# Optimization experiments

Measured on AMD Instinct MI355X. Metric: run time of the kernel, lower is better.

The kernel has to match this reference:

```python
import jax, jax.numpy as jnp
import numpy as np

N, E, XD, H, L, G, C = 20000, 320000, 128, 256, 4, 128, 10
EPS = 1e-5


def setup_inputs() -> dict:
    key = jax.random.key(0)
    ks = jax.random.split(key, 24)
    s = 0.05
    inp = {
        "x": jax.random.normal(ks[0], (N, XD), jnp.float32),
        "edge_index": jax.random.randint(ks[1], (2, E), 0, N, jnp.int32),
        "batch": jnp.sort(jax.random.randint(ks[2], (N,), 0, G, jnp.int32)),
        "encW": jax.random.normal(ks[3], (XD, H), jnp.float32) * s,
        "encB": jnp.zeros((H,), jnp.float32),
        "convW": jax.random.normal(ks[4], (L, H, H), jnp.float32) * s,
        "convB": jnp.zeros((L, H), jnp.float32),
        "bnG": jnp.ones((L, H), jnp.float32),
        "bnB": jnp.zeros((L, H), jnp.float32),
        "fcW1": jax.random.normal(ks[5], (H, H), jnp.float32) * s,
        "fcB1": jnp.zeros((H,), jnp.float32),
        "fcG1": jnp.ones((H,), jnp.float32),
        "fcBe1": jnp.zeros((H,), jnp.float32),
        "fcW2": jax.random.normal(ks[6], (H, H), jnp.float32) * s,
        "fcB2": jnp.zeros((H,), jnp.float32),
        "fcG2": jnp.ones((H,), jnp.float32),
        "fcBe2": jnp.zeros((H,), jnp.float32),
        "fcW3": jax.random.normal(ks[7], (H, C), jnp.float32) * s,
        "fcB3": jnp.zeros((C,), jnp.float32),
    }
    return inp


def _bn(h, g, b):
    # BatchNorm1d, training-mode batch statistics (biased var), eps=1e-5
    m = h.mean(0)
    v = h.var(0)
    return g * (h - m) * jax.lax.rsqrt(v + EPS) + b


def _forward(x, edge_index, batch, encW, encB, convW, convB, bnG, bnB,
             fcW1, fcB1, fcG1, fcBe1, fcW2, fcB2, fcG2, fcBe2, fcW3, fcB3):
    src, dst = edge_index[0], edge_index[1]
    # GCN symmetric normalization with implicit self-loops (fill value 1)
    deg = jax.ops.segment_sum(jnp.ones((E,), x.dtype), dst, num_segments=N) + 1.0
    dinv = jax.lax.rsqrt(deg)
    enorm = (dinv[src] * dinv[dst])[:, None]       # [E,1]
    self_norm = (dinv * dinv)[:, None]             # [N,1] self-loop coeff

    h = x @ encW + encB                            # node encoder
    for i in range(L):
        t = h @ convW[i]                           # GCNConv linear (no bias)
        agg = jax.ops.segment_sum(t[src] * enorm, dst, num_segments=N)
        t = agg + t * self_norm + convB[i]         # aggregate + self loop + bias
        h = jax.nn.relu(_bn(t, bnG[i], bnB[i]))    # dropout is identity (eval)

    # global mean pool over graph ids
    sums = jax.ops.segment_sum(h, batch, num_segments=G)
    cnts = jax.ops.segment_sum(jnp.ones((N,), h.dtype), batch, num_segments=G)
    g = sums / jnp.maximum(cnts, 1.0)[:, None]     # [G,H]

    # fc_out: MLP(Linear->BN->ReLU->Linear) -> BN -> Linear
    m = jax.nn.relu(_bn(g @ fcW1 + fcB1, fcG1, fcBe1)) @ fcW2 + fcB2
    m = _bn(m, fcG2, fcBe2)
    return m @ fcW3 + fcB3                         # [G,C]


def reference(x, edge_index, batch, encW, encB, convW, convB, bnG, bnB,
              fcW1, fcB1, fcG1, fcBe1, fcW2, fcB2, fcG2, fcBe2, fcW3, fcB3):
    return _forward(x, edge_index, batch, encW, encB, convW, convB, bnG, bnB,
                    fcW1, fcB1, fcG1, fcBe1, fcW2, fcB2, fcG2, fcBe2, fcW3, fcB3)
```

## Files before the change

### kernel.cpp

```cpp
#include <hip/hip_runtime.h>
#include <hip/hip_bf16.h>
#include <cstddef>

#define N_NODES 20000
#define N_EDGES 320000
#define XDIM 128
#define H 256
#define LAYERS 4
#define G_GRAPHS 128
#define C_OUT 10
#define EPS_BN 1e-5f
#define NSLOT 64
#define NB 8

typedef __attribute__((ext_vector_type(8))) short short8;
typedef __attribute__((ext_vector_type(4))) float f32x4;
typedef __attribute__((address_space(3))) unsigned int lds_u32;
typedef const __attribute__((address_space(1))) unsigned int glob_u32;

__global__ void hist_kernel(const int* __restrict__ dst, int* __restrict__ cnt, int E) {
    int e = blockIdx.x * blockDim.x + threadIdx.x;
    if (e < E) atomicAdd(&cnt[dst[e]], 1);
}

__global__ void scan_kernel(const int* __restrict__ cnt, int* __restrict__ rowstart,
                            float* __restrict__ dinv, int N) {
    __shared__ int partial[1024];
    int tid = threadIdx.x;
    int chunk = (N + 1023) / 1024;
    int start = tid * chunk;
    int lsum = 0;
    for (int i = 0; i < chunk; ++i) {
        int idx = start + i;
        if (idx < N) {
            int c = cnt[idx];
            dinv[idx] = 1.0f / sqrtf((float)c + 1.0f);
            lsum += c;
        }
    }
    partial[tid] = lsum;
    __syncthreads();
    for (int off = 1; off < 1024; off <<= 1) {
        int v = (tid >= off) ? partial[tid - off] : 0;
        __syncthreads();
        partial[tid] += v;
        __syncthreads();
    }
    int run = (tid == 0) ? 0 : partial[tid - 1];
    for (int i = 0; i < chunk; ++i) {
        int idx = start + i;
        if (idx < N) { rowstart[idx] = run; run += cnt[idx]; }
    }
    if (tid == 1023) rowstart[N] = partial[1023];
}

__global__ void fill_kernel(const int* __restrict__ src, const int* __restrict__ dst,
                            const int* __restrict__ rowstart, int* __restrict__ cursor,
                            const float* __restrict__ dinv,
                            int* __restrict__ csr_src, float* __restrict__ csr_w, int E) {
    int e = blockIdx.x * blockDim.x + threadIdx.x;
    if (e < E) {
        int s = src[e], d = dst[e];
        int pos = rowstart[d] + atomicAdd(&cursor[d], 1);
        csr_src[pos] = s;
        csr_w[pos] = dinv[s] * dinv[d];
    }
}

__global__ void cast_bf16_kernel(const float* __restrict__ in, __hip_bfloat16* __restrict__ out, int n) {
    int i = blockIdx.x * blockDim.x + threadIdx.x;
    if (i < n) out[i] = __float2bfloat16(in[i]);
}

__global__ void tcast_kernel(const float* __restrict__ in, __hip_bfloat16* __restrict__ out,
                             int R, int C, int layers) {
    int i = blockIdx.x * blockDim.x + threadIdx.x;
    int per = R * C;
    if (i >= per * layers) return;
    int l = i / per, rem = i - l * per;
    int r = rem / C, c = rem - r * C;
    out[(size_t)l * per + (size_t)c * R + r] = __float2bfloat16(in[i]);
}

__device__ __forceinline__ short bf16bits(float x) {
    __hip_bfloat16 b = __float2bfloat16(x);
    return *(short*)&b;
}

template <int K, bool FUSE_BN>
__global__ __launch_bounds__(256) void gemm_bf16_kernel(
    const void* __restrict__ Ain,
    const __hip_bfloat16* __restrict__ BT,
    const float* __restrict__ bias,
    const float* __restrict__ bnsc,
    const float* __restrict__ bnsh,
    __hip_bfloat16* __restrict__ Cbf,
    int M, int Nn) {
    __shared__ short As[64 * 32];
    __shared__ short Bs[128 * 32];
    const short* Ash = (const short*)Ain;
    const float* Af = (const float*)Ain;
    const short* Bsh = (const short*)BT;
    int tid = threadIdx.x;
    int lane = tid & 63;
    int wave = tid >> 6;
    int quad = lane >> 4;
    int lr = lane & 15;
    int wm = (wave & 1) * 32;
    int wn = (wave >> 1) * 64;
    int Mblk = blockIdx.x * 64;
    int Nblk = blockIdx.y * 128;

    f32x4 acc[2][4];
#pragma unroll
    for (int i = 0; i < 2; ++i)
#pragma unroll
        for (int j = 0; j < 4; ++j) acc[i][j] = (f32x4){0.f, 0.f, 0.f, 0.f};

    int srow = tid >> 2, sqs = tid & 3;
    int sqg = sqs ^ ((srow >> 1) & 3);
    int arow = Mblk + srow; if (arow >= M) arow = M - 1;
    int s1 = 256 + tid;
    int brow0 = Nblk + (tid >> 2);
    int qg0 = sqg;
    int brow1 = Nblk + (s1 >> 2);
    int qg1 = (s1 & 3) ^ (((s1 >> 2) >> 1) & 3);

    for (int k0 = 0; k0 < K; k0 += 32) {
        int kc = k0 + sqg * 8;
        __builtin_amdgcn_global_load_lds((glob_u32*)(Bsh + (size_t)brow0 * K + k0 + qg0 * 8),
                                         (lds_u32*)Bs + wave * 256, 16, 0, 0);
        __builtin_amdgcn_global_load_lds((glob_u32*)(Bsh + (size_t)brow1 * K + k0 + qg1 * 8),
                                         (lds_u32*)Bs + 1024 + wave * 256, 16, 0, 0);
        if (FUSE_BN) {
            float4 v0 = *(const float4*)(Af + (size_t)arow * K + kc);
            float4 v1 = *(const float4*)(Af + (size_t)arow * K + kc + 4);
            float4 c0 = *(const float4*)(bnsc + kc);
            float4 c1 = *(const float4*)(bnsc + kc + 4);
            float4 h0 = *(const float4*)(bnsh + kc);
            float4 h1 = *(const float4*)(bnsh + kc + 4);
            short8 pk;
            pk[0] = bf16bits(fmaxf(v0.x * c0.x + h0.x, 0.f));
            pk[1] = bf16bits(fmaxf(v0.y * c0.y + h0.y, 0.f));
            pk[2] = bf16bits(fmaxf(v0.z * c0.z + h0.z, 0.f));
            pk[3] = bf16bits(fmaxf(v0.w * c0.w + h0.w, 0.f));
            pk[4] = bf16bits(fmaxf(v1.x * c1.x + h1.x, 0.f));
            pk[5] = bf16bits(fmaxf(v1.y * c1.y + h1.y, 0.f));
            pk[6] = bf16bits(fmaxf(v1.z * c1.z + h1.z, 0.f));
            pk[7] = bf16bits(fmaxf(v1.w * c1.w + h1.w, 0.f));
            *(short8*)&As[srow * 32 + sqs * 8] = pk;
        } else {
            __builtin_amdgcn_global_load_lds((glob_u32*)(Ash + (size_t)arow * K + kc),
                                             (lds_u32*)As + wave * 256, 16, 0, 0);
        }
        __syncthreads();
        short8 af[2], bfr[4];
#pragma unroll
        for (int mi = 0; mi < 2; ++mi) {
            int r = wm + mi * 16 + lr;
            af[mi] = *(const short8*)&As[r * 32 + (quad ^ ((r >> 1) & 3)) * 8];
        }
#pragma unroll
        for (int ni = 0; ni < 4; ++ni) {
            int r = wn + ni * 16 + lr;
            bfr[ni] = *(const short8*)&Bs[r * 32 + (quad ^ ((r >> 1) & 3)) * 8];
        }
#pragma unroll
        for (int mi = 0; mi < 2; ++mi)
#pragma unroll
            for (int ni = 0; ni < 4; ++ni)
                acc[mi][ni] = __builtin_amdgcn_mfma_f32_16x16x32_bf16(af[mi], bfr[ni], acc[mi][ni], 0, 0, 0);
        __syncthreads();
    }
#pragma unroll
    for (int mi = 0; mi < 2; ++mi) {
#pragma unroll
        for (int r = 0; r < 4; ++r) {
            int m = Mblk + wm + mi * 16 + quad * 4 + r;
            if (m < M) {
#pragma unroll
                for (int ni = 0; ni < 4; ++ni) {
                    int n = Nblk + wn + ni * 16 + lr;
                    float v = acc[mi][ni][r];
                    if (bias) v += bias[n];
                    Cbf[(size_t)m * Nn + n] = __float2bfloat16(v);
                }
            }
        }
    }
}

__global__ __launch_bounds__(256) void agg_kernel(const __hip_bfloat16* __restrict__ t,
                           const int* __restrict__ rowstart,
                           const int* __restrict__ csr_src,
                           const float* __restrict__ csr_w,
                           const float* __restrict__ dinv,
                           const float* __restrict__ convB,
                           float* __restrict__ out,
                           float* __restrict__ spart,
                           int N) {
    __shared__ float red[4][256];
    int tid = threadIdx.x;
    int wave = tid >> 6;
    int lane = tid & 63;
    int sub = lane >> 5;
    int hl = lane & 31;
    int stream = wave * 2 + sub;
    int c0 = hl * 8;
    const ushort* tp = (const ushort*)t;
    float sv = 0.f, sq = 0.f;
    int n0 = blockIdx.x * NB;
#pragma unroll 1
    for (int it = 0; it < NB; ++it) {
        int n = n0 + it;
        int s = rowstart[n], e = rowstart[n + 1];
        float a[8] = {};
#pragma unroll 1
        for (int j0 = s; j0 < e; j0 += 16) {
#pragma unroll
            for (int u = 0; u < 2; ++u) {
                int j = j0 + u * 8 + stream;
                int idx = n; float w = 0.f;
                if (j < e) { idx = csr_src[j]; w = csr_w[j]; }
                uint4 v = *(const uint4*)(tp + (size_t)idx * H + c0);
                a[0] += __uint_as_float(v.x << 16) * w;
                a[1] += __uint_as_float(v.x & 0xffff0000u) * w;
                a[2] += __uint_as_float(v.y << 16) * w;
                a[3] += __uint_as_float(v.y & 0xffff0000u) * w;
                a[4] += __uint_as_float(v.z << 16) * w;
                a[5] += __uint_as_float(v.z & 0xffff0000u) * w;
                a[6] += __uint_as_float(v.w << 16) * w;
                a[7] += __uint_as_float(v.w & 0xffff0000u) * w;
            }
        }
#pragma unroll
        for (int k = 0; k < 8; ++k) a[k] += __shfl_xor(a[k], 32);
        if (sub == 0) {
            *(float4*)&red[wave][c0] = make_float4(a[0], a[1], a[2], a[3]);
            *(float4*)&red[wave][c0 + 4] = make_float4(a[4], a[5], a[6], a[7]);
        }
        __syncthreads();
        int c = tid;
        float val = red[0][c] + red[1][c] + red[2][c] + red[3][c];
        float dn = dinv[n];
        val += __bfloat162float(t[(size_t)n * H + c]) * (dn * dn) + convB[c];
        out[(size_t)n * H + c] = val;
        sv += val; sq += val * val;
        __syncthreads();
    }
    float* sp = spart + (size_t)(blockIdx.x & (NSLOT - 1)) * (2 * H);
    atomicAdd(&sp[tid], sv);
    atomicAdd(&sp[H + tid], sq);
}

__global__ void make_bnparams_kernel(const float* __restrict__ spart,
                                     const float* __restrict__ gamma,
                                     const float* __restrict__ beta,
                                     float* __restrict__ sc, float* __restrict__ sh) {
    int c = threadIdx.x;
    float s = 0.f, s2 = 0.f;
#pragma unroll 8
    for (int i = 0; i < NSLOT; ++i) {
        s  += spart[(size_t)i * (2 * H) + c];
        s2 += spart[(size_t)i * (2 * H) + H + c];
    }
    float invN = 1.0f / (float)N_NODES;
    float mean = s * invN;
    float var = s2 * invN - mean * mean;
    float k = gamma[c] / sqrtf(var + EPS_BN);
    sc[c] = k;
    sh[c] = beta[c] - mean * k;
}

__global__ __launch_bounds__(256) void pool_kernel(const float* __restrict__ t2,
                            const int* __restrict__ batch,
                            const float* __restrict__ sc, const float* __restrict__ sh,
                            float* __restrict__ g, int N) {
    __shared__ float4 red[4][64];
    int gid = blockIdx.x;
    int lo = 0, hi = N;
    while (lo < hi) { int mid = (lo + hi) >> 1; if (batch[mid] < gid) lo = mid + 1; else hi = mid; }
    int s = lo;
    lo = s; hi = N;
    while (lo < hi) { int mid = (lo + hi) >> 1; if (batch[mid] < gid + 1) lo = mid + 1; else hi = mid; }
    int e = lo;
    int wave = threadIdx.x >> 6;
    int lane = threadIdx.x & 63;
    float4 scv = *(const float4*)(sc + lane * 4);
    float4 shv = *(const float4*)(sh + lane * 4);
    float a0 = 0.f, a1 = 0.f, a2 = 0.f, a3 = 0.f;
    for (int r = s + wave; r < e; r += 4) {
        float4 v = *(const float4*)(t2 + (size_t)r * H + lane * 4);
        a0 += __bfloat162float(__float2bfloat16(fmaxf(v.x * scv.x + shv.x, 0.f)));
        a1 += __bfloat162float(__float2bfloat16(fmaxf(v.y * scv.y + shv.y, 0.f)));
        a2 += __bfloat162float(__float2bfloat16(fmaxf(v.z * scv.z + shv.z, 0.f)));
        a3 += __bfloat162float(__float2bfloat16(fmaxf(v.w * scv.w + shv.w, 0.f)));
    }
    red[wave][lane] = make_float4(a0, a1, a2, a3);
    __syncthreads();
    int c = threadIdx.x;
    const float* rf = (const float*)red;
    float sum = rf[c] + rf[256 + c] + rf[512 + c] + rf[768 + c];
    g[(size_t)gid * H + c] = sum / fmaxf((float)(e - s), 1.0f);
}

template <int K, int NN>
__global__ __launch_bounds__(256) void fc_lds_kernel(const float* __restrict__ in,
                                                     const float* __restrict__ W,
                                                     const float* __restrict__ b,
                                                     float* __restrict__ out) {
    __shared__ float row[K];
    int g = blockIdx.x;
    for (int k = threadIdx.x; k < K; k += 256) row[k] = in[(size_t)g * K + k];
    __syncthreads();
    int hc = threadIdx.x;
    if (hc < NN) {
        float acc = b[hc];
#pragma unroll
        for (int k = 0; k < K; ++k) acc += row[k] * W[k * NN + hc];
        out[(size_t)g * NN + hc] = acc;
    }
}

__global__ void fc_out_kernel(const float* __restrict__ in, const float* __restrict__ W,
                              const float* __restrict__ b, float* __restrict__ out) {
    int t = blockIdx.x * blockDim.x + threadIdx.x;
    if (t >= G_GRAPHS * C_OUT) return;
    int g = t / C_OUT, c = t % C_OUT;
    float acc = b[c];
#pragma unroll 16
    for (int k = 0; k < H; ++k) acc += in[(size_t)g * H + k] * W[k * C_OUT + c];
    out[t] = acc;
}

__global__ void bn_head_kernel(const float* __restrict__ in, const float* __restrict__ gamma,
                               const float* __restrict__ beta, float* __restrict__ out,
                               int Grows, int relu) {
    int c = blockIdx.x;
    int r = threadIdx.x;
    __shared__ float red[G_GRAPHS];
    float v = in[r * H + c];
    red[r] = v;
    __syncthreads();
    for (int off = G_GRAPHS / 2; off > 0; off >>= 1) {
        if (r < off) red[r] += red[r + off];
        __syncthreads();
    }
    float mean = red[0] / (float)Grows;
    __syncthreads();
    float d = v - mean;
    red[r] = d * d;
    __syncthreads();
    for (int off = G_GRAPHS / 2; off > 0; off >>= 1) {
        if (r < off) red[r] += red[r + off];
        __syncthreads();
    }
    float var = red[0] / (float)Grows;
    float y = gamma[c] * d / sqrtf(var + EPS_BN) + beta[c];
    if (relu) y = fmaxf(y, 0.f);
    out[r * H + c] = y;
}

extern "C" void kernel_launch(void* const* d_in, const int* in_sizes, int n_in,
                              void* d_out, int out_size, void* d_ws, size_t ws_size,
                              hipStream_t stream) {
    const float* x     = (const float*)d_in[0];
    const int*   edge  = (const int*)d_in[1];
    const int*   batch = (const int*)d_in[2];
    const float* encW  = (const float*)d_in[3];
    const float* encB  = (const float*)d_in[4];
    const float* convW = (const float*)d_in[5];
    const float* convB = (const float*)d_in[6];
    const float* bnG   = (const float*)d_in[7];
    const float* bnB   = (const float*)d_in[8];
    const float* fcW1  = (const float*)d_in[9];
    const float* fcB1  = (const float*)d_in[10];
    const float* fcG1  = (const float*)d_in[11];
    const float* fcBe1 = (const float*)d_in[12];
    const float* fcW2  = (const float*)d_in[13];
    const float* fcB2  = (const float*)d_in[14];
    const float* fcG2  = (const float*)d_in[15];
    const float* fcBe2 = (const float*)d_in[16];
    const float* fcW3  = (const float*)d_in[17];
    const float* fcB3  = (const float*)d_in[18];
    float* out = (float*)d_out;

    const int* srcIdx = edge;
    const int* dstIdx = edge + N_EDGES;

    char* base = (char*)d_ws;
    size_t off = 0;
    auto alloc = [&](size_t bytes) -> void* {
        void* p = base + off;
        off = (off + bytes + 255) & ~(size_t)255;
        return p;
    };
    int*   cnt      = (int*)alloc(N_NODES * 4);
    int*   cursor   = (int*)alloc(N_NODES * 4);
    int*   rowstart = (int*)alloc((N_NODES + 1) * 4);
    float* dinv     = (float*)alloc(N_NODES * 4);
    int*   csr_src  = (int*)alloc(N_EDGES * 4);
    float* csr_w    = (float*)alloc(N_EDGES * 4);
    float* spart    = (float*)alloc((size_t)LAYERS * NSLOT * 2 * H * 4);
    float* scbuf    = (float*)alloc((size_t)LAYERS * H * 4);
    float* shbuf    = (float*)alloc((size_t)LAYERS * H * 4);
    __hip_bfloat16* xbf    = (__hip_bfloat16*)alloc((size_t)N_NODES * XDIM * 2);
    __hip_bfloat16* encWT  = (__hip_bfloat16*)alloc((size_t)H * XDIM * 2);
    __hip_bfloat16* convWT = (__hip_bfloat16*)alloc((size_t)LAYERS * H * H * 2);
    __hip_bfloat16* hbf    = (__hip_bfloat16*)alloc((size_t)N_NODES * H * 2);
    __hip_bfloat16* tbf    = (__hip_bfloat16*)alloc((size_t)N_NODES * H * 2);
    float* t2buf = (float*)alloc((size_t)N_NODES * H * 4);
    float* gpool = (float*)alloc(G_GRAPHS * H * 4);
    float* m1    = (float*)alloc(G_GRAPHS * H * 4);
    float* m2    = (float*)alloc(G_GRAPHS * H * 4);

    hipMemsetAsync(cnt, 0, (size_t)((char*)rowstart - (char*)cnt), stream);
    hipMemsetAsync(spart, 0, (size_t)LAYERS * NSLOT * 2 * H * 4, stream);

    hist_kernel<<<(N_EDGES + 255) / 256, 256, 0, stream>>>(dstIdx, cnt, N_EDGES);
    scan_kernel<<<1, 1024, 0, stream>>>(cnt, rowstart, dinv, N_NODES);
    fill_kernel<<<(N_EDGES + 255) / 256, 256, 0, stream>>>(srcIdx, dstIdx, rowstart, cursor,
                                                           dinv, csr_src, csr_w, N_EDGES);

    cast_bf16_kernel<<<(N_NODES * XDIM + 255) / 256, 256, 0, stream>>>(x, xbf, N_NODES * XDIM);
    tcast_kernel<<<(XDIM * H + 255) / 256, 256, 0, stream>>>(encW, encWT, XDIM, H, 1);
    tcast_kernel<<<(LAYERS * H * H + 255) / 256, 256, 0, stream>>>(convW, convWT, H, H, LAYERS);

    dim3 gridG((N_NODES + 63) / 64, H / 128);
    gemm_bf16_kernel<XDIM, false><<<gridG, 256, 0, stream>>>(
        xbf, encWT, encB, nullptr, nullptr, hbf, N_NODES, H);

    for (int l = 0; l < LAYERS; ++l) {
        float* spartL = spart + (size_t)l * NSLOT * 2 * H;
        if (l == 0) {
            gemm_bf16_kernel<H, false><<<gridG, 256, 0, stream>>>(
                hbf, convWT + (size_t)l * H * H, nullptr, nullptr, nullptr, tbf, N_NODES, H);
        } else {
            gemm_bf16_kernel<H, true><<<gridG, 256, 0, stream>>>(
                t2buf, convWT + (size_t)l * H * H, nullptr,
                scbuf + (size_t)(l - 1) * H, shbuf + (size_t)(l - 1) * H, tbf, N_NODES, H);
        }
        agg_kernel<<<N_NODES / NB, 256, 0, stream>>>(tbf, rowstart, csr_src, csr_w, dinv,
                                                     convB + l * H, t2buf, spartL, N_NODES);
        make_bnparams_kernel<<<1, H, 0, stream>>>(spartL, bnG + l * H, bnB + l * H,
                                                  scbuf + (size_t)l * H, shbuf + (size_t)l * H);
    }

    pool_kernel<<<G_GRAPHS, 256, 0, stream>>>(t2buf, batch,
                                              scbuf + (size_t)(LAYERS - 1) * H,
                                              shbuf + (size_t)(LAYERS - 1) * H, gpool, N_NODES);

    fc_lds_kernel<H, H><<<G_GRAPHS, 256, 0, stream>>>(gpool, fcW1, fcB1, m1);
    bn_head_kernel<<<H, G_GRAPHS, 0, stream>>>(m1, fcG1, fcBe1, m1, G_GRAPHS, 1);
    fc_lds_kernel<H, H><<<G_GRAPHS, 256, 0, stream>>>(m1, fcW2, fcB2, m2);
    bn_head_kernel<<<H, G_GRAPHS, 0, stream>>>(m2, fcG2, fcBe2, m2, G_GRAPHS, 0);
    fc_out_kernel<<<(G_GRAPHS * C_OUT + 255) / 256, 256, 0, stream>>>(m2, fcW3, fcB3, out);
}
```

Before: 453.4 us.

## Double-buffer GEMM tiles, fold BN-param computation into consumers, merge cast kernels

The GEMM now uses two LDS buffers so the next K-tile's global loads are issued before the current tile's MFMAs, with one barrier per iteration instead of two. The separate make_bnparams kernel is removed: each GEMM block and pool block recomputes the BN scale and shift from the partial sums into shared memory. The three cast/transpose kernels are merged into one prep launch. Together these cut launch count and load latency, at the cost of redundant per-block reduction work over NSLOT partials and doubled LDS use.

```diff
diff --git a/kernel.cpp b/kernel.cpp
--- a/kernel.cpp
+++ b/kernel.cpp
@@ -67,19 +67,27 @@
     }
 }
 
-__global__ void cast_bf16_kernel(const float* __restrict__ in, __hip_bfloat16* __restrict__ out, int n) {
+__global__ void prep_kernel(const float* __restrict__ x, const float* __restrict__ encW,
+                            const float* __restrict__ convW,
+                            __hip_bfloat16* __restrict__ xbf,
+                            __hip_bfloat16* __restrict__ encWT,
+                            __hip_bfloat16* __restrict__ convWT) {
     int i = blockIdx.x * blockDim.x + threadIdx.x;
-    if (i < n) out[i] = __float2bfloat16(in[i]);
-}
-
-__global__ void tcast_kernel(const float* __restrict__ in, __hip_bfloat16* __restrict__ out,
-                             int R, int C, int layers) {
-    int i = blockIdx.x * blockDim.x + threadIdx.x;
-    int per = R * C;
-    if (i >= per * layers) return;
-    int l = i / per, rem = i - l * per;
-    int r = rem / C, c = rem - r * C;
-    out[(size_t)l * per + (size_t)c * R + r] = __float2bfloat16(in[i]);
+    const int nx = N_NODES * XDIM;
+    const int ne = XDIM * H;
+    const int nc = LAYERS * H * H;
+    if (i < nx) {
+        xbf[i] = __float2bfloat16(x[i]);
+    } else if (i < nx + ne) {
+        int j = i - nx;
+        int r = j / H, c = j - r * H;
+        encWT[c * XDIM + r] = __float2bfloat16(encW[j]);
+    } else if (i < nx + ne + nc) {
+        int j = i - nx - ne;
+        int l = j / (H * H), rem = j - l * (H * H);
+        int r = rem / H, c = rem - r * H;
+        convWT[(size_t)l * H * H + c * H + r] = __float2bfloat16(convW[j]);
+    }
 }
 
 __device__ __forceinline__ short bf16bits(float x) {
@@ -92,12 +100,15 @@
     const void* __restrict__ Ain,
     const __hip_bfloat16* __restrict__ BT,
     const float* __restrict__ bias,
-    const float* __restrict__ bnsc,
-    const float* __restrict__ bnsh,
+    const float* __restrict__ spart,
+    const float* __restrict__ gamma,
+    const float* __restrict__ beta,
     __hip_bfloat16* __restrict__ Cbf,
     int M, int Nn) {
-    __shared__ short As[64 * 32];
-    __shared__ short Bs[128 * 32];
+    __shared__ short As[2][64 * 32];
+    __shared__ short Bs[2][128 * 32];
+    __shared__ float scs[H];
+    __shared__ float shs[H];
     const short* Ash = (const short*)Ain;
     const float* Af = (const float*)Ain;
     const short* Bsh = (const short*)BT;
@@ -126,51 +137,85 @@
     int brow1 = Nblk + (s1 >> 2);
     int qg1 = (s1 & 3) ^ (((s1 >> 2) >> 1) & 3);
 
-    for (int k0 = 0; k0 < K; k0 += 32) {
+    if (FUSE_BN) {
+        int c = tid;
+        float s = 0.f, s2 = 0.f;
+#pragma unroll 8
+        for (int i = 0; i < NSLOT; ++i) {
+            s  += spart[(size_t)i * (2 * H) + c];
+            s2 += spart[(size_t)i * (2 * H) + H + c];
+        }
+        float invN = 1.0f / (float)N_NODES;
+        float mean = s * invN;
+        float var = s2 * invN - mean * mean;
+        float kk = gamma[c] / sqrtf(var + EPS_BN);
+        scs[c] = kk;
+        shs[c] = beta[c] - mean * kk;
+        __syncthreads();
+    }
+
+    float4 ra0, ra1;
+    auto loadA_f = [&](int k0) {
         int kc = k0 + sqg * 8;
+        ra0 = *(const float4*)(Af + (size_t)arow * K + kc);
+        ra1 = *(const float4*)(Af + (size_t)arow * K + kc + 4);
+    };
+    auto storeA_f = [&](int buf, int k0) {
+        int kc = k0 + sqg * 8;
+        float4 c0 = *(const float4*)&scs[kc];
+        float4 c1 = *(const float4*)&scs[kc + 4];
+        float4 h0 = *(const float4*)&shs[kc];
+        float4 h1 = *(const float4*)&shs[kc + 4];
+        short8 pk;
+        pk[0] = bf16bits(fmaxf(ra0.x * c0.x + h0.x, 0.f));
+        pk[1] = bf16bits(fmaxf(ra0.y * c0.y + h0.y, 0.f));
+        pk[2] = bf16bits(fmaxf(ra0.z * c0.z + h0.z, 0.f));
+        pk[3] = bf16bits(fmaxf(ra0.w * c0.w + h0.w, 0.f));
+        pk[4] = bf16bits(fmaxf(ra1.x * c1.x + h1.x, 0.f));
+        pk[5] = bf16bits(fmaxf(ra1.y * c1.y + h1.y, 0.f));
+        pk[6] = bf16bits(fmaxf(ra1.z * c1.z + h1.z, 0.f));
+        pk[7] = bf16bits(fmaxf(ra1.w * c1.w + h1.w, 0.f));
+        *(short8*)&As[buf][srow * 32 + sqs * 8] = pk;
+    };
+    auto stageA_async = [&](int buf, int k0) {
+        __builtin_amdgcn_global_load_lds((glob_u32*)(Ash + (size_t)arow * K + k0 + sqg * 8),
+                                         (lds_u32*)&As[buf][0] + wave * 256, 16, 0, 0);
+    };
+    auto stageB = [&](int buf, int k0) {
         __builtin_amdgcn_global_load_lds((glob_u32*)(Bsh + (size_t)brow0 * K + k0 + qg0 * 8),
-                                         (lds_u32*)Bs + wave * 256, 16, 0, 0);
+                                         (lds_u32*)&Bs[buf][0] + wave * 256, 16, 0, 0);
         __builtin_amdgcn_global_load_lds((glob_u32*)(Bsh + (size_t)brow1 * K + k0 + qg1 * 8),
-                                         (lds_u32*)Bs + 1024 + wave * 256, 16, 0, 0);
-        if (FUSE_BN) {
-            float4 v0 = *(const float4*)(Af + (size_t)arow * K + kc);
-            float4 v1 = *(const float4*)(Af + (size_t)arow * K + kc + 4);
-            float4 c0 = *(const float4*)(bnsc + kc);
-            float4 c1 = *(const float4*)(bnsc + kc + 4);
-            float4 h0 = *(const float4*)(bnsh + kc);
-            float4 h1 = *(const float4*)(bnsh + kc + 4);
-            short8 pk;
-            pk[0] = bf16bits(fmaxf(v0.x * c0.x + h0.x, 0.f));
-            pk[1] = bf16bits(fmaxf(v0.y * c0.y + h0.y, 0.f));
-            pk[2] = bf16bits(fmaxf(v0.z * c0.z + h0.z, 0.f));
-            pk[3] = bf16bits(fmaxf(v0.w * c0.w + h0.w, 0.f));
-            pk[4] = bf16bits(fmaxf(v1.x * c1.x + h1.x, 0.f));
-            pk[5] = bf16bits(fmaxf(v1.y * c1.y + h1.y, 0.f));
-            pk[6] = bf16bits(fmaxf(v1.z * c1.z + h1.z, 0.f));
-            pk[7] = bf16bits(fmaxf(v1.w * c1.w + h1.w, 0.f));
-            *(short8*)&As[srow * 32 + sqs * 8] = pk;
-        } else {
-            __builtin_amdgcn_global_load_lds((glob_u32*)(Ash + (size_t)arow * K + kc),
-                                             (lds_u32*)As + wave * 256, 16, 0, 0);
-        }
-        __syncthreads();
+                                         (lds_u32*)&Bs[buf][0] + 1024 + wave * 256, 16, 0, 0);
+    };
+
+    constexpr int NK = K / 32;
+    if (FUSE_BN) loadA_f(0); else stageA_async(0, 0);
+    stageB(0, 0);
+#pragma unroll
+    for (int k = 0; k < NK; ++k) {
+        int buf = k & 1;
+        if (FUSE_BN) storeA_f(buf, k * 32);
+        __syncthreads();
+        if (k + 1 < NK) {
+            if (FUSE_BN) loadA_f((k + 1) * 32); else stageA_async(buf ^ 1, (k + 1) * 32);
+            stageB(buf ^ 1, (k + 1) * 32);
+        }
         short8 af[2], bfr[4];
 #pragma unroll
         for (int mi = 0; mi < 2; ++mi) {
             int r = wm + mi * 16 + lr;
-            af[mi] = *(const short8*)&As[r * 32 + (quad ^ ((r >> 1) & 3)) * 8];
+            af[mi] = *(const short8*)&As[buf][r * 32 + (quad ^ ((r >> 1) & 3)) * 8];
         }
 #pragma unroll
         for (int ni = 0; ni < 4; ++ni) {
             int r = wn + ni * 16 + lr;
-            bfr[ni] = *(const short8*)&Bs[r * 32 + (quad ^ ((r >> 1) & 3)) * 8];
+            bfr[ni] = *(const short8*)&Bs[buf][r * 32 + (quad ^ ((r >> 1) & 3)) * 8];
         }
 #pragma unroll
         for (int mi = 0; mi < 2; ++mi)
 #pragma unroll
             for (int ni = 0; ni < 4; ++ni)
                 acc[mi][ni] = __builtin_amdgcn_mfma_f32_16x16x32_bf16(af[mi], bfr[ni], acc[mi][ni], 0, 0, 0);
-        __syncthreads();
     }
 #pragma unroll
     for (int mi = 0; mi < 2; ++mi) {
@@ -253,30 +298,31 @@
     atomicAdd(&sp[H + tid], sq);
 }
 
-__global__ void make_bnparams_kernel(const float* __restrict__ spart,
-                                     const float* __restrict__ gamma,
-                                     const float* __restrict__ beta,
-                                     float* __restrict__ sc, float* __restrict__ sh) {
-    int c = threadIdx.x;
-    float s = 0.f, s2 = 0.f;
-#pragma unroll 8
-    for (int i = 0; i < NSLOT; ++i) {
-        s  += spart[(size_t)i * (2 * H) + c];
-        s2 += spart[(size_t)i * (2 * H) + H + c];
-    }
-    float invN = 1.0f / (float)N_NODES;
-    float mean = s * invN;
-    float var = s2 * invN - mean * mean;
-    float k = gamma[c] / sqrtf(var + EPS_BN);
-    sc[c] = k;
-    sh[c] = beta[c] - mean * k;
-}
-
 __global__ __launch_bounds__(256) void pool_kernel(const float* __restrict__ t2,
                             const int* __restrict__ batch,
-                            const float* __restrict__ sc, const float* __restrict__ sh,
+                            const float* __restrict__ spart,
+                            const float* __restrict__ gamma,
+                            const float* __restrict__ beta,
                             float* __restrict__ g, int N) {
     __shared__ float4 red[4][64];
+    __shared__ float scs[H];
+    __shared__ float shs[H];
+    {
+        int c = threadIdx.x;
+        float s = 0.f, s2 = 0.f;
+#pragma unroll 8
+        for (int i = 0; i < NSLOT; ++i) {
+            s  += spart[(size_t)i * (2 * H) + c];
+            s2 += spart[(size_t)i * (2 * H) + H + c];
+        }
+        float invN = 1.0f / (float)N_NODES;
+        float mean = s * invN;
+        float var = s2 * invN - mean * mean;
+        float kk = gamma[c] / sqrtf(var + EPS_BN);
+        scs[c] = kk;
+        shs[c] = beta[c] - mean * kk;
+    }
+    __syncthreads();
     int gid = blockIdx.x;
     int lo = 0, hi = N;
     while (lo < hi) { int mid = (lo + hi) >> 1; if (batch[mid] < gid) lo = mid + 1; else hi = mid; }
@@ -286,8 +332,8 @@
     int e = lo;
     int wave = threadIdx.x >> 6;
     int lane = threadIdx.x & 63;
-    float4 scv = *(const float4*)(sc + lane * 4);
-    float4 shv = *(const float4*)(sh + lane * 4);
+    float4 scv = *(const float4*)&scs[lane * 4];
+    float4 shv = *(const float4*)&shs[lane * 4];
     float a0 = 0.f, a1 = 0.f, a2 = 0.f, a3 = 0.f;
     for (int r = s + wave; r < e; r += 4) {
         float4 v = *(const float4*)(t2 + (size_t)r * H + lane * 4);
@@ -402,8 +448,6 @@
     int*   csr_src  = (int*)alloc(N_EDGES * 4);
     float* csr_w    = (float*)alloc(N_EDGES * 4);
     float* spart    = (float*)alloc((size_t)LAYERS * NSLOT * 2 * H * 4);
-    float* scbuf    = (float*)alloc((size_t)LAYERS * H * 4);
-    float* shbuf    = (float*)alloc((size_t)LAYERS * H * 4);
     __hip_bfloat16* xbf    = (__hip_bfloat16*)alloc((size_t)N_NODES * XDIM * 2);
     __hip_bfloat16* encWT  = (__hip_bfloat16*)alloc((size_t)H * XDIM * 2);
     __hip_bfloat16* convWT = (__hip_bfloat16*)alloc((size_t)LAYERS * H * H * 2);
@@ -422,33 +466,35 @@
     fill_kernel<<<(N_EDGES + 255) / 256, 256, 0, stream>>>(srcIdx, dstIdx, rowstart, cursor,
                                                            dinv, csr_src, csr_w, N_EDGES);
 
-    cast_bf16_kernel<<<(N_NODES * XDIM + 255) / 256, 256, 0, stream>>>(x, xbf, N_NODES * XDIM);
-    tcast_kernel<<<(XDIM * H + 255) / 256, 256, 0, stream>>>(encW, encWT, XDIM, H, 1);
-    tcast_kernel<<<(LAYERS * H * H + 255) / 256, 256, 0, stream>>>(convW, convWT, H, H, LAYERS);
+    {
+        int total = N_NODES * XDIM + XDIM * H + LAYERS * H * H;
+        prep_kernel<<<(total + 255) / 256, 256, 0, stream>>>(x, encW, convW, xbf, encWT, convWT);
+    }
 
     dim3 gridG((N_NODES + 63) / 64, H / 128);
     gemm_bf16_kernel<XDIM, false><<<gridG, 256, 0, stream>>>(
-        xbf, encWT, encB, nullptr, nullptr, hbf, N_NODES, H);
+        xbf, encWT, encB, nullptr, nullptr, nullptr, hbf, N_NODES, H);
 
     for (int l = 0; l < LAYERS; ++l) {
         float* spartL = spart + (size_t)l * NSLOT * 2 * H;
         if (l == 0) {
             gemm_bf16_kernel<H, false><<<gridG, 256, 0, stream>>>(
-                hbf, convWT + (size_t)l * H * H, nullptr, nullptr, nullptr, tbf, N_NODES, H);
+                hbf, convWT + (size_t)l * H * H, nullptr, nullptr, nullptr, nullptr,
+                tbf, N_NODES, H);
         } else {
+            float* spartP = spart + (size_t)(l - 1) * NSLOT * 2 * H;
             gemm_bf16_kernel<H, true><<<gridG, 256, 0, stream>>>(
                 t2buf, convWT + (size_t)l * H * H, nullptr,
-                scbuf + (size_t)(l - 1) * H, shbuf + (size_t)(l - 1) * H, tbf, N_NODES, H);
+                spartP, bnG + (size_t)(l - 1) * H, bnB + (size_t)(l - 1) * H,
+                tbf, N_NODES, H);
         }
         agg_kernel<<<N_NODES / NB, 256, 0, stream>>>(tbf, rowstart, csr_src, csr_w, dinv,
                                                      convB + l * H, t2buf, spartL, N_NODES);
-        make_bnparams_kernel<<<1, H, 0, stream>>>(spartL, bnG + l * H, bnB + l * H,
-                                                  scbuf + (size_t)l * H, shbuf + (size_t)l * H);
-    }
-
-    pool_kernel<<<G_GRAPHS, 256, 0, stream>>>(t2buf, batch,
-                                              scbuf + (size_t)(LAYERS - 1) * H,
-                                              shbuf + (size_t)(LAYERS - 1) * H, gpool, N_NODES);
+    }
+
+    pool_kernel<<<G_GRAPHS, 256, 0, stream>>>(
+        t2buf, batch, spart + (size_t)(LAYERS - 1) * NSLOT * 2 * H,
+        bnG + (size_t)(LAYERS - 1) * H, bnB + (size_t)(LAYERS - 1) * H, gpool, N_NODES);
 
     fc_lds_kernel<H, H><<<G_GRAPHS, 256, 0, stream>>>(gpool, fcW1, fcB1, m1);
     bn_head_kernel<<<H, G_GRAPHS, 0, stream>>>(m1, fcG1, fcBe1, m1, G_GRAPHS, 1);
```

Result: no change. 446.6 us (-1.5%).
